# Performance work log

Hardware: AMD Instinct MI355X
Metric: run time of the kernel (lower is better)

## Reference

```python
import jax, jax.numpy as jnp
import numpy as np
from jax import lax

B, T, K = 256, 512, 128


def setup_inputs() -> dict:
    key = jax.random.key(0)
    k1, k2, k3, k4 = jax.random.split(key, 4)
    tag_weights = jax.random.normal(k1, (B, T, K), dtype=jnp.float32)
    transition_weights = jax.random.normal(k2, (K, K), dtype=jnp.float32)
    # gold tags; -1 marks an unannotated (unclamped) position, as in partial CRF
    gold = jax.random.randint(k3, (B, T), -1, K)
    lengths = jax.random.randint(k4, (B,), 1, T + 1)
    return {"tag_weights": tag_weights, "transition_weights": transition_weights,
            "gold": gold, "lengths": lengths}


def _log_partition(tag_weights, transition, lengths):
    # tag_weights: [B,T,K], transition: [K,K] (trans[i,j] = score i->j), lengths: [B]
    Tt = tag_weights.shape[1]
    alpha0 = tag_weights[:, 0]                      # [B,K]
    emits = jnp.moveaxis(tag_weights[:, 1:], 1, 0)  # [T-1,B,K]
    ts = jnp.arange(1, Tt)

    def step(alpha, xs):
        emit, t = xs
        # stable logsumexp over previous tag i: [B,K_prev,1] + [1,K_prev,K_cur]
        new = jax.nn.logsumexp(alpha[:, :, None] + transition[None], axis=1) + emit
        # freeze alpha for finished sequences (t >= length)
        alpha = jnp.where((t < lengths)[:, None], new, alpha)
        return alpha, None

    alphaT, _ = lax.scan(step, alpha0, (emits, ts))
    return jax.nn.logsumexp(alphaT, axis=-1)  # [B]


def _clamp(tag_weights, gold, lengths):
    Bt, Tt, Kt = tag_weights.shape
    ar = jnp.arange(Kt)
    valid = jnp.arange(Tt)[None, :] < lengths[:, None]            # [B,T]
    allow = (gold[:, :, None] == ar[None, None, :]) | (gold[:, :, None] < 0)  # [B,T,K]
    # within length: only gold tag (or all if gold<0) allowed; beyond length the
    # recurrence is frozen so those positions are left unmasked (unused).
    mask = jnp.where(allow | ~valid[:, :, None], 0.0, -jnp.inf)
    return tag_weights + mask


def reference(tag_weights, transition_weights, gold, lengths):
    clamped = _clamp(tag_weights, gold, lengths)
    loss = (_log_partition(tag_weights, transition_weights, lengths)
            - _log_partition(clamped, transition_weights, lengths))
    return loss.mean()  # reduction='mean'
```

## Files before the change

### kernel.cpp

```cpp
#include <hip/hip_runtime.h>
#include <hip/hip_bf16.h>

#define B_DIM 256
#define T_DIM 512
#define K_DIM 128

typedef float f32x4 __attribute__((ext_vector_type(4)));

__global__ __attribute__((amdgpu_flat_work_group_size(256, 256)))
__attribute__((amdgpu_waves_per_eu(2, 2)))
void crf_pass_kernel(
    const float* __restrict__ tw,
    const float* __restrict__ trans,
    const int*   __restrict__ gold,
    const int*   __restrict__ lengths,
    float*       __restrict__ wsv)
{
    const int bid = blockIdx.x;
    const int b = bid & (B_DIM - 1);
    const bool clamp = bid >= B_DIM;
    const int tid = threadIdx.x;
    const int k = tid >> 1;
    const int h = tid & 1;
    const int j0 = h * 64;

    __shared__ __align__(16) float qbuf[2][K_DIM];
    __shared__ float rsum[2][4];

    f32x4 E0, E1, E2, E3, E4, E5, E6, E7, E8, E9, E10, E11, E12, E13, E14, E15;
#define LOADE(n) { \
        const float* tp = &trans[(j0 + 4*(n)) * K_DIM + k]; \
        E##n.x = __expf(tp[0 * K_DIM]); \
        E##n.y = __expf(tp[1 * K_DIM]); \
        E##n.z = __expf(tp[2 * K_DIM]); \
        E##n.w = __expf(tp[3 * K_DIM]); }
    LOADE(0); LOADE(1); LOADE(2); LOADE(3);
    LOADE(4); LOADE(5); LOADE(6); LOADE(7);
    LOADE(8); LOADE(9); LOADE(10); LOADE(11);
    LOADE(12); LOADE(13); LOADE(14); LOADE(15);
#undef LOADE
    asm volatile("" : "+v"(E0), "+v"(E1), "+v"(E2), "+v"(E3),
                      "+v"(E4), "+v"(E5), "+v"(E6), "+v"(E7),
                      "+v"(E8), "+v"(E9), "+v"(E10), "+v"(E11),
                      "+v"(E12), "+v"(E13), "+v"(E14), "+v"(E15));

    const int len = lengths[b];
    const float* twb = tw + (size_t)b * T_DIM * K_DIM;
    const int* gb = gold + b * T_DIM;

    float m = 0.0f;
    {
        float e0 = twb[k];
        int g = clamp ? gb[0] : -1;
        float q = __expf(e0);
        if (g >= 0 && g != k) q = 0.0f;
        if (h == 0) qbuf[0][k] = q;
        float v = q;
#pragma unroll
        for (int off = 2; off <= 32; off <<= 1) v += __shfl_xor(v, off);
        if ((tid & 63) == 0) rsum[0][tid >> 6] = v;
    }
    __syncthreads();

    float ec[4]; int gc[4];
#pragma unroll
    for (int i = 0; i < 4; ++i) {
        int t = 1 + i; if (t > T_DIM - 1) t = T_DIM - 1;
        ec[i] = twb[t * K_DIM + k];
        gc[i] = clamp ? gb[t] : -1;
    }

    for (int t0 = 1; t0 < len; t0 += 4) {
        float en[4]; int gn[4];
#pragma unroll
        for (int i = 0; i < 4; ++i) {
            int t = t0 + 4 + i; if (t > T_DIM - 1) t = T_DIM - 1;
            en[i] = twb[t * K_DIM + k];
            gn[i] = clamp ? gb[t] : -1;
        }

#pragma unroll
        for (int i = 0; i < 4; ++i) {
            const int t = t0 + i;
            if (t < len) {
                const int cur = (t - 1) & 1, nxt = t & 1;
                const f32x4* qv = (const f32x4*)&qbuf[cur][j0];
                float R = (rsum[cur][0] + rsum[cur][1]) + (rsum[cur][2] + rsum[cur][3]);
                float x = __expf(ec[i]);
                float a0 = 0.f, a1 = 0.f, a2 = 0.f, a3 = 0.f;
#define FMA4(n) { f32x4 pj = qv[n]; \
                  a0 = fmaf(pj.x, E##n.x, a0); a1 = fmaf(pj.y, E##n.y, a1); \
                  a2 = fmaf(pj.z, E##n.z, a2); a3 = fmaf(pj.w, E##n.w, a3); }
                FMA4(0);  FMA4(1);  FMA4(2);  FMA4(3);
                FMA4(4);  FMA4(5);  FMA4(6);  FMA4(7);
                FMA4(8);  FMA4(9);  FMA4(10); FMA4(11);
                FMA4(12); FMA4(13); FMA4(14); FMA4(15);
#undef FMA4
                float s_half = (a0 + a1) + (a2 + a3);
                float s = s_half + __shfl_xor(s_half, 1);
                float qn = s * x * __builtin_amdgcn_rcpf(R);
                int g = gc[i];
                if (g >= 0 && g != k) qn = 0.0f;
                m += __logf(R);
                if (h == 0) qbuf[nxt][k] = qn;
                float v = qn;
#pragma unroll
                for (int off = 2; off <= 32; off <<= 1) v += __shfl_xor(v, off);
                if ((tid & 63) == 0) rsum[nxt][tid >> 6] = v;
            }
            __syncthreads();
        }
#pragma unroll
        for (int i = 0; i < 4; ++i) { ec[i] = en[i]; gc[i] = gn[i]; }
    }

    if (tid == 0) {
        const int cur = (len - 1) & 1;
        float R = (rsum[cur][0] + rsum[cur][1]) + (rsum[cur][2] + rsum[cur][3]);
        wsv[bid] = m + __logf(R);
    }
}

__global__ void crf_finalize(const float* __restrict__ wsv, float* __restrict__ out)
{
    const int tid = threadIdx.x;
    float d = wsv[tid] - wsv[B_DIM + tid];
#pragma unroll
    for (int off = 32; off; off >>= 1) d += __shfl_xor(d, off);
    __shared__ float red[4];
    if ((tid & 63) == 0) red[tid >> 6] = d;
    __syncthreads();
    if (tid == 0) out[0] = (red[0] + red[1] + red[2] + red[3]) * (1.0f / (float)B_DIM);
}

extern "C" void kernel_launch(void* const* d_in, const int* in_sizes, int n_in,
                              void* d_out, int out_size, void* d_ws, size_t ws_size,
                              hipStream_t stream)
{
    const float* tw      = (const float*)d_in[0];
    const float* trans   = (const float*)d_in[1];
    const int*   gold    = (const int*)d_in[2];
    const int*   lengths = (const int*)d_in[3];
    float* wsv = (float*)d_ws;
    float* out = (float*)d_out;

    crf_pass_kernel<<<2 * B_DIM, 256, 0, stream>>>(tw, trans, gold, lengths, wsv);
    crf_finalize<<<1, B_DIM, 0, stream>>>(wsv, out);
}
```

Measured before the change: 375.1 us.

## Fuse unclamped and clamped CRF recurrences into one block per sequence

Each block now runs both the unclamped and the clamped forward recurrences for one sequence, sharing the exp-transition registers and emission/gold loads, and launches half as many blocks. The per-step normaliser is now computed redundantly by each thread from the shared q vector, instead of through a cross-wave shuffle reduction written to shared memory, which removes that reduction from the serial critical path. The cost is twice the LDS reads and FMAs per step in each block, plus half the grid parallelism on 256 CUs. The waves-per-EU hint is also loosened.

```diff
diff --git a/kernel.cpp b/kernel.cpp
--- a/kernel.cpp
+++ b/kernel.cpp
@@ -8,7 +8,7 @@
 typedef float f32x4 __attribute__((ext_vector_type(4)));
 
 __global__ __attribute__((amdgpu_flat_work_group_size(256, 256)))
-__attribute__((amdgpu_waves_per_eu(2, 2)))
+__attribute__((amdgpu_waves_per_eu(1, 2)))
 void crf_pass_kernel(
     const float* __restrict__ tw,
     const float* __restrict__ trans,
@@ -16,16 +16,15 @@
     const int*   __restrict__ lengths,
     float*       __restrict__ wsv)
 {
-    const int bid = blockIdx.x;
-    const int b = bid & (B_DIM - 1);
-    const bool clamp = bid >= B_DIM;
+    const int b = blockIdx.x;
     const int tid = threadIdx.x;
     const int k = tid >> 1;
     const int h = tid & 1;
     const int j0 = h * 64;
 
-    __shared__ __align__(16) float qbuf[2][K_DIM];
-    __shared__ float rsum[2][4];
+    __shared__ __align__(16) float qU[2][K_DIM];
+    __shared__ __align__(16) float qC[2][K_DIM];
+    __shared__ float redU[4], redC[4];
 
     f32x4 E0, E1, E2, E3, E4, E5, E6, E7, E8, E9, E10, E11, E12, E13, E14, E15;
 #define LOADE(n) { \
@@ -48,17 +47,15 @@
     const float* twb = tw + (size_t)b * T_DIM * K_DIM;
     const int* gb = gold + b * T_DIM;
 
-    float m = 0.0f;
+    float mU = 0.0f, mC = 0.0f;
+    float lastU, lastC;
     {
         float e0 = twb[k];
-        int g = clamp ? gb[0] : -1;
-        float q = __expf(e0);
-        if (g >= 0 && g != k) q = 0.0f;
-        if (h == 0) qbuf[0][k] = q;
-        float v = q;
-#pragma unroll
-        for (int off = 2; off <= 32; off <<= 1) v += __shfl_xor(v, off);
-        if ((tid & 63) == 0) rsum[0][tid >> 6] = v;
+        int g = gb[0];
+        float u = __expf(e0);
+        float c = (g < 0 || g == k) ? u : 0.0f;
+        if (h == 0) { qU[0][k] = u; qC[0][k] = c; }
+        lastU = u; lastC = c;
     }
     __syncthreads();
 
@@ -67,7 +64,7 @@
     for (int i = 0; i < 4; ++i) {
         int t = 1 + i; if (t > T_DIM - 1) t = T_DIM - 1;
         ec[i] = twb[t * K_DIM + k];
-        gc[i] = clamp ? gb[t] : -1;
+        gc[i] = gb[t];
     }
 
     for (int t0 = 1; t0 < len; t0 += 4) {
@@ -76,7 +73,7 @@
         for (int i = 0; i < 4; ++i) {
             int t = t0 + 4 + i; if (t > T_DIM - 1) t = T_DIM - 1;
             en[i] = twb[t * K_DIM + k];
-            gn[i] = clamp ? gb[t] : -1;
+            gn[i] = gb[t];
         }
 
 #pragma unroll
@@ -84,29 +81,33 @@
             const int t = t0 + i;
             if (t < len) {
                 const int cur = (t - 1) & 1, nxt = t & 1;
-                const f32x4* qv = (const f32x4*)&qbuf[cur][j0];
-                float R = (rsum[cur][0] + rsum[cur][1]) + (rsum[cur][2] + rsum[cur][3]);
+                const f32x4* au = (const f32x4*)&qU[cur][j0];
+                const f32x4* ac = (const f32x4*)&qC[cur][j0];
                 float x = __expf(ec[i]);
-                float a0 = 0.f, a1 = 0.f, a2 = 0.f, a3 = 0.f;
-#define FMA4(n) { f32x4 pj = qv[n]; \
-                  a0 = fmaf(pj.x, E##n.x, a0); a1 = fmaf(pj.y, E##n.y, a1); \
-                  a2 = fmaf(pj.z, E##n.z, a2); a3 = fmaf(pj.w, E##n.w, a3); }
-                FMA4(0);  FMA4(1);  FMA4(2);  FMA4(3);
-                FMA4(4);  FMA4(5);  FMA4(6);  FMA4(7);
-                FMA4(8);  FMA4(9);  FMA4(10); FMA4(11);
-                FMA4(12); FMA4(13); FMA4(14); FMA4(15);
-#undef FMA4
-                float s_half = (a0 + a1) + (a2 + a3);
-                float s = s_half + __shfl_xor(s_half, 1);
-                float qn = s * x * __builtin_amdgcn_rcpf(R);
+                f32x4 sU = {0.f,0.f,0.f,0.f}, rU = {0.f,0.f,0.f,0.f};
+                f32x4 sC = {0.f,0.f,0.f,0.f}, rC = {0.f,0.f,0.f,0.f};
+#define Q4(n) { f32x4 a = au[n], c = ac[n]; \
+                sU = __builtin_elementwise_fma(a, E##n, sU); rU += a; \
+                sC = __builtin_elementwise_fma(c, E##n, sC); rC += c; }
+                Q4(0);  Q4(1);  Q4(2);  Q4(3);
+                Q4(4);  Q4(5);  Q4(6);  Q4(7);
+                Q4(8);  Q4(9);  Q4(10); Q4(11);
+                Q4(12); Q4(13); Q4(14); Q4(15);
+#undef Q4
+                float su = (sU.x + sU.y) + (sU.z + sU.w);
+                float ru = (rU.x + rU.y) + (rU.z + rU.w);
+                float sc = (sC.x + sC.y) + (sC.z + sC.w);
+                float rc = (rC.x + rC.y) + (rC.z + rC.w);
+                su += __shfl_xor(su, 1); ru += __shfl_xor(ru, 1);
+                sc += __shfl_xor(sc, 1); rc += __shfl_xor(rc, 1);
+                float qu_ = su * x * __builtin_amdgcn_rcpf(ru);
+                float qc_ = sc * x * __builtin_amdgcn_rcpf(rc);
                 int g = gc[i];
-                if (g >= 0 && g != k) qn = 0.0f;
-                m += __logf(R);
-                if (h == 0) qbuf[nxt][k] = qn;
-                float v = qn;
-#pragma unroll
-                for (int off = 2; off <= 32; off <<= 1) v += __shfl_xor(v, off);
-                if ((tid & 63) == 0) rsum[nxt][tid >> 6] = v;
+                if (g >= 0 && g != k) qc_ = 0.0f;
+                mU += __logf(ru);
+                mC += __logf(rc);
+                if (h == 0) { qU[nxt][k] = qu_; qC[nxt][k] = qc_; }
+                lastU = qu_; lastC = qc_;
             }
             __syncthreads();
         }
@@ -114,17 +115,26 @@
         for (int i = 0; i < 4; ++i) { ec[i] = en[i]; gc[i] = gn[i]; }
     }
 
+    float vU = (h == 0) ? lastU : 0.0f;
+    float vC = (h == 0) ? lastC : 0.0f;
+#pragma unroll
+    for (int off = 1; off < 64; off <<= 1) {
+        vU += __shfl_xor(vU, off);
+        vC += __shfl_xor(vC, off);
+    }
+    if ((tid & 63) == 0) { redU[tid >> 6] = vU; redC[tid >> 6] = vC; }
+    __syncthreads();
     if (tid == 0) {
-        const int cur = (len - 1) & 1;
-        float R = (rsum[cur][0] + rsum[cur][1]) + (rsum[cur][2] + rsum[cur][3]);
-        wsv[bid] = m + __logf(R);
+        float SU = (redU[0] + redU[1]) + (redU[2] + redU[3]);
+        float SC = (redC[0] + redC[1]) + (redC[2] + redC[3]);
+        wsv[b] = (mU + __logf(SU)) - (mC + __logf(SC));
     }
 }
 
 __global__ void crf_finalize(const float* __restrict__ wsv, float* __restrict__ out)
 {
     const int tid = threadIdx.x;
-    float d = wsv[tid] - wsv[B_DIM + tid];
+    float d = wsv[tid];
 #pragma unroll
     for (int off = 32; off; off >>= 1) d += __shfl_xor(d, off);
     __shared__ float red[4];
@@ -144,6 +154,6 @@
     float* wsv = (float*)d_ws;
     float* out = (float*)d_out;
 
-    crf_pass_kernel<<<2 * B_DIM, 256, 0, stream>>>(tw, trans, gold, lengths, wsv);
+    crf_pass_kernel<<<B_DIM, 256, 0, stream>>>(tw, trans, gold, lengths, wsv);
     crf_finalize<<<1, B_DIM, 0, stream>>>(wsv, out);
 }
```

After: 389.8 us. 3.9% more time.
